# Kernel tuning notes

Hardware: AMD Instinct MI355X
Metric: run time of the kernel (lower is better)

## Reference

```python
import jax, jax.numpy as jnp
import numpy as np

B = 2
E = [16384, 32768, 65536, 131072]
CONVS = [256, 128, 64, 32, 8]


def mesh_conv(x, gemm, W, b):
    # x: (B, C, E); gemm: (E, 4) neighbor edge indices; W: (Cout, Cin, 5)
    n = x[:, :, gemm]  # (B, C, E, 4) irregular gather over mesh topology
    f1, f2, f3, f4 = n[..., 0], n[..., 1], n[..., 2], n[..., 3]
    # MeshCNN symmetric functions over the 4 gemm neighbors
    G = jnp.stack([x, f1 + f3, f2 + f4, jnp.abs(f1 - f3), jnp.abs(f2 - f4)], axis=-1)  # (B,C,E,5)
    return jnp.einsum('bces,ocs->boe', G, W) + b[None, :, None]


def inorm(x, eps=1e-5):
    # InstanceNorm2d, affine=False: normalize per (sample, channel) over edge dim
    m = jnp.mean(x, axis=2, keepdims=True)
    v = jnp.var(x, axis=2, keepdims=True)
    return (x - m) * jax.lax.rsqrt(v + eps)


def setup_inputs() -> dict:
    key = jax.random.key(0)
    ks = iter(jax.random.split(key, 64))
    inp = {}
    inp['fe'] = jax.random.normal(next(ks), (B, CONVS[0], E[0]), jnp.float32)
    for i in range(3):
        inp[f'skip{i}'] = jax.random.normal(next(ks), (B, CONVS[i + 1], E[i + 1]), jnp.float32)
    for r in range(4):
        inp[f'gemm{r}'] = jax.random.randint(next(ks), (E[r], 4), 0, E[r], jnp.int32)
    for i in range(3):
        inp[f'unpool{i}'] = jax.random.randint(next(ks), (E[i + 1],), 0, E[i], jnp.int32)

    def mk(cout, cin, name):
        inp[f'W{name}'] = jax.random.normal(next(ks), (cout, cin, 5), jnp.float32) * (1.0 / np.sqrt(5.0 * cin))
        inp[f'b{name}'] = jnp.zeros((cout,), jnp.float32)

    for i in range(3):
        mk(CONVS[i + 1], CONVS[i], f'up{i}')
        mk(CONVS[i + 1], CONVS[i + 1], f'c{i}')
    mk(CONVS[4], CONVS[3], 'upf')
    mk(CONVS[4], CONVS[4], 'cf')
    return inp


def reference(fe, skip0, skip1, skip2, gemm0, gemm1, gemm2, gemm3,
              unpool0, unpool1, unpool2,
              Wup0, bup0, Wc0, bc0, Wup1, bup1, Wc1, bc1, Wup2, bup2, Wc2, bc2,
              Wupf, bupf, Wcf, bcf):
    gemms = [gemm0, gemm1, gemm2, gemm3]
    unpools = [unpool0, unpool1, unpool2]
    skips = [skip0, skip1, skip2]
    Wups = [Wup0, Wup1, Wup2]
    bups = [bup0, bup1, bup2]
    Wcs = [Wc0, Wc1, Wc2]
    bcs = [bc0, bc1, bc2]
    x = fe
    for i in range(3):  # fixed small loop over decoder stages
        x1 = mesh_conv(x, gemms[i], Wups[i], bups[i])      # up_conv at coarse res
        x1 = x1[:, :, unpools[i]]                          # MeshUnpool: copy to fine edges
        x1 = x1 + skips[i]                                 # transfer_data skip add
        x1 = mesh_conv(x1, gemms[i + 1], Wcs[i], bcs[i])   # conv1 at fine res
        x = jax.nn.relu(inorm(x1))                         # InstanceNorm + ReLU (blocks=0)
    # final UpConv: no unroll, no skip
    x1 = mesh_conv(x, gemms[3], Wupf, bupf)
    x1 = mesh_conv(x1, gemms[3], Wcf, bcf)
    return jax.nn.relu(inorm(x1))
```

## Files before the change

kernel.cpp:

```cpp
#include <hip/hip_runtime.h>
#include <hip/hip_bf16.h>
#include <cstdint>
#include <cstddef>


typedef short s16x8 __attribute__((ext_vector_type(8)));
typedef unsigned short u16x8 __attribute__((ext_vector_type(8)));
typedef float f32x4 __attribute__((ext_vector_type(4)));

__device__ __forceinline__ float bfbits2f(unsigned short u) {
    unsigned int x = ((unsigned int)u) << 16;
    float f; __builtin_memcpy(&f, &x, sizeof(f)); return f;
}
__device__ __forceinline__ unsigned short f2bfbits(float f) {
    __hip_bfloat16 h = __float2bfloat16(f);
    unsigned short u; __builtin_memcpy(&u, &h, sizeof(u)); return u;
}

__global__ __launch_bounds__(256) void k_transpose_in(
    const float* __restrict__ in, unsigned short* __restrict__ out, int C, int E)
{
    __shared__ float tile[64][65];
    const int e0 = blockIdx.x * 64;
    const int c0 = blockIdx.y * 64;
    const int b  = blockIdx.z;
    const float* inb = in + (size_t)b * C * E;
    const int l = threadIdx.x % 64;
    const int g = threadIdx.x / 64;
#pragma unroll
    for (int i = 0; i < 16; ++i) {
        const int c = i * 4 + g;
        tile[c][l] = inb[(size_t)(c0 + c) * E + e0 + l];
    }
    __syncthreads();
    unsigned short* outb = out + (size_t)b * E * C;
#pragma unroll
    for (int i = 0; i < 16; ++i) {
        const int e = i * 4 + g;
        outb[(size_t)(e0 + e) * C + c0 + l] = f2bfbits(tile[l][e]);
    }
}

__global__ __launch_bounds__(256) void k_prep_b(
    const float* __restrict__ W, unsigned short* __restrict__ Bp, int C, int OP, int OL)
{
    const int p = blockIdx.x * 256 + threadIdx.x;
    const int total = 5 * C * OP;
    if (p >= total) return;
    const int j = p & 7;
    const int t = p >> 3;
    const int o = t % OP;
    const int kk = t / OP;
    const int k = kk * 8 + j;
    const int s = k / C;
    const int c = k - s * C;
    Bp[p] = (o < OL) ? f2bfbits(W[((size_t)o * C + c) * 5 + s]) : (unsigned short)0;
}

__global__ __launch_bounds__(256) void k_prep_w(
    const float* __restrict__ W, float* __restrict__ Wt, int C, int O)
{
    const int idx = blockIdx.x * 256 + threadIdx.x;
    const int total = C * 5 * O;
    if (idx >= total) return;
    const int k = idx / O;
    const int o = idx % O;
    const int c = k / 5;
    const int s = k - 5 * c;
    Wt[idx] = W[((size_t)o * C + c) * 5 + s];
}

template<int C, int O, bool STATS, int OW = O>
__global__ __launch_bounds__(256) void k_conv_mfma(
    const unsigned short* __restrict__ x, const int* __restrict__ gm,
    const unsigned short* __restrict__ Bp, const float* __restrict__ bias,
    unsigned short* __restrict__ out, float* __restrict__ stats, int E)
{
    constexpr int NT    = O / 16;
    constexpr int ITS   = C / 32;
    constexpr int OCT   = C / 8;
    constexpr int ITERS = (64 * OCT) / 256;
    constexpr int PAD   = 8;
    constexpr int RW    = C + PAD;
    constexpr bool PAIRED = (C <= 128);
    constexpr int SLOTS = PAIRED ? 2 : 1;
    static_assert(C % 32 == 0 && O % 16 == 0, "bad cfg");

    __shared__ unsigned short smem[SLOTS][64][RW];
    __shared__ int gis[64][4];

    const int tid  = threadIdx.x;
    const int wave = tid >> 6;
    const int lane = tid & 63;
    const int m    = lane & 15;
    const int kq   = lane >> 4;
    const int b    = blockIdx.y;
    const int e0   = blockIdx.x * 64;
    const unsigned short* xb = x + (size_t)b * E * C;
    const s16x8* Bp8 = reinterpret_cast<const s16x8*>(Bp);

    if (tid < 64)
        *reinterpret_cast<int4*>(gis[tid]) =
            *reinterpret_cast<const int4*>(gm + 4 * (size_t)(e0 + tid));

    f32x4 acc[NT];
#pragma unroll
    for (int nt = 0; nt < NT; ++nt) acc[nt] = (f32x4){0.f, 0.f, 0.f, 0.f};

    auto mfma_seg = [&](int slot, int s) {
#pragma unroll
        for (int it = 0; it < ITS; ++it) {
            const s16x8 afrag = *reinterpret_cast<const s16x8*>(
                &smem[slot][wave * 16 + m][it * 32 + kq * 8]);
            const int kkb = s * OCT + it * 4 + kq;
#pragma unroll
            for (int nt = 0; nt < NT; ++nt) {
                const s16x8 bfrag = Bp8[(size_t)kkb * O + nt * 16 + m];
                acc[nt] = __builtin_amdgcn_mfma_f32_16x16x32_bf16(afrag, bfrag, acc[nt], 0, 0, 0);
            }
        }
    };

#pragma unroll
    for (int i = 0; i < ITERS; ++i) {
        const int task = i * 256 + tid;
        const int r    = task / OCT;
        const int oct  = task % OCT;
        const u16x8 v = *reinterpret_cast<const u16x8*>(
            xb + (size_t)(e0 + r) * C + oct * 8);
        *reinterpret_cast<u16x8*>(&smem[0][r][oct * 8]) = v;
    }
    __syncthreads();
    mfma_seg(0, 0);
    __syncthreads();

    if constexpr (PAIRED) {
#pragma unroll
        for (int i = 0; i < ITERS; ++i) {
            const int task = i * 256 + tid;
            const int r    = task / OCT;
            const int oct  = task % OCT;
            const u16x8 a = *reinterpret_cast<const u16x8*>(
                xb + (size_t)gis[r][0] * C + oct * 8);
            const u16x8 c = *reinterpret_cast<const u16x8*>(
                xb + (size_t)gis[r][2] * C + oct * 8);
            u16x8 vs, vd;
#pragma unroll
            for (int j = 0; j < 8; ++j) {
                const float fa = bfbits2f(a[j]);
                const float fc = bfbits2f(c[j]);
                vs[j] = f2bfbits(fa + fc);
                vd[j] = f2bfbits(fabsf(fa - fc));
            }
            *reinterpret_cast<u16x8*>(&smem[0][r][oct * 8]) = vs;
            *reinterpret_cast<u16x8*>(&smem[SLOTS - 1][r][oct * 8]) = vd;
        }
        __syncthreads();
        mfma_seg(0, 1);
        mfma_seg(SLOTS - 1, 3);
        __syncthreads();
#pragma unroll
        for (int i = 0; i < ITERS; ++i) {
            const int task = i * 256 + tid;
            const int r    = task / OCT;
            const int oct  = task % OCT;
            const u16x8 a = *reinterpret_cast<const u16x8*>(
                xb + (size_t)gis[r][1] * C + oct * 8);
            const u16x8 c = *reinterpret_cast<const u16x8*>(
                xb + (size_t)gis[r][3] * C + oct * 8);
            u16x8 vs, vd;
#pragma unroll
            for (int j = 0; j < 8; ++j) {
                const float fa = bfbits2f(a[j]);
                const float fc = bfbits2f(c[j]);
                vs[j] = f2bfbits(fa + fc);
                vd[j] = f2bfbits(fabsf(fa - fc));
            }
            *reinterpret_cast<u16x8*>(&smem[0][r][oct * 8]) = vs;
            *reinterpret_cast<u16x8*>(&smem[SLOTS - 1][r][oct * 8]) = vd;
        }
        __syncthreads();
        mfma_seg(0, 2);
        mfma_seg(SLOTS - 1, 4);
    } else {
#pragma unroll
        for (int s = 1; s <= 4; ++s) {
            const int ia = (s == 1 || s == 3) ? 0 : 1;
#pragma unroll
            for (int i = 0; i < ITERS; ++i) {
                const int task = i * 256 + tid;
                const int r    = task / OCT;
                const int oct  = task % OCT;
                const u16x8 a = *reinterpret_cast<const u16x8*>(
                    xb + (size_t)gis[r][ia] * C + oct * 8);
                const u16x8 c = *reinterpret_cast<const u16x8*>(
                    xb + (size_t)gis[r][ia + 2] * C + oct * 8);
                u16x8 v;
#pragma unroll
                for (int j = 0; j < 8; ++j) {
                    const float fa = bfbits2f(a[j]);
                    const float fc = bfbits2f(c[j]);
                    v[j] = f2bfbits((s < 3) ? (fa + fc) : fabsf(fa - fc));
                }
                *reinterpret_cast<u16x8*>(&smem[0][r][oct * 8]) = v;
            }
            __syncthreads();
            mfma_seg(0, s);
            if (s != 4) __syncthreads();
        }
    }

    const int ebase = e0 + wave * 16 + kq * 4;
    float ssum[NT], ssq[NT];
#pragma unroll
    for (int nt = 0; nt < NT; ++nt) { ssum[nt] = 0.f; ssq[nt] = 0.f; }
#pragma unroll
    for (int nt = 0; nt < NT; ++nt) {
        const int o = nt * 16 + m;
        if (o < OW) {
            const float bo = bias[o];
#pragma unroll
            for (int r = 0; r < 4; ++r) {
                const float z = acc[nt][r] + bo;
                out[((size_t)b * E + (ebase + r)) * OW + o] = f2bfbits(z);
                ssum[nt] += z; ssq[nt] += z * z;
            }
        }
    }

    if constexpr (STATS) {
        __shared__ float ls[4][2][O];
#pragma unroll
        for (int nt = 0; nt < NT; ++nt) {
            float s = ssum[nt], q = ssq[nt];
            s += __shfl_xor(s, 16); s += __shfl_xor(s, 32);
            q += __shfl_xor(q, 16); q += __shfl_xor(q, 32);
            if (kq == 0) { ls[wave][0][nt * 16 + m] = s; ls[wave][1][nt * 16 + m] = q; }
        }
        __syncthreads();
        if (tid < O) {
            const float S = ls[0][0][tid] + ls[1][0][tid] + ls[2][0][tid] + ls[3][0][tid];
            const float Q = ls[0][1][tid] + ls[1][1][tid] + ls[2][1][tid] + ls[3][1][tid];
            atomicAdd(&stats[((size_t)b * O + tid) * 2], S);
            atomicAdd(&stats[((size_t)b * O + tid) * 2 + 1], Q);
        }
    }
}

template<int C, int O, bool STATS>
__global__ __launch_bounds__(256) void k_conv_small(
    const unsigned short* __restrict__ x, const int* __restrict__ gm,
    const float* __restrict__ Wt, const float* __restrict__ bias,
    unsigned short* __restrict__ out, float* __restrict__ stats, int E)
{
    static_assert(O == 8 && C % 8 == 0, "bad cfg");
    __shared__ float ls[2 * O];
    const int tid = threadIdx.x;
    if constexpr (STATS) {
        if (tid < 2 * O) ls[tid] = 0.f;
        __syncthreads();
    }
    const int b = blockIdx.y;
    const int e = blockIdx.x * 256 + tid;
    const unsigned short* xb = x + (size_t)b * E * C;
    const int4 gi = *reinterpret_cast<const int4*>(gm + 4 * (size_t)e);
    const unsigned short* rp[5] = {
        xb + (size_t)e * C, xb + (size_t)gi.x * C, xb + (size_t)gi.y * C,
        xb + (size_t)gi.z * C, xb + (size_t)gi.w * C };

    float acc[O];
#pragma unroll
    for (int o = 0; o < O; ++o) acc[o] = bias[o];

#pragma unroll
    for (int c = 0; c < C; c += 8) {
        u16x8 rv[5];
#pragma unroll
        for (int k = 0; k < 5; ++k) rv[k] = *reinterpret_cast<const u16x8*>(rp[k] + c);
#pragma unroll
        for (int cc = 0; cc < 8; ++cc) {
            const float x0 = bfbits2f(rv[0][cc]);
            const float f1 = bfbits2f(rv[1][cc]);
            const float f2 = bfbits2f(rv[2][cc]);
            const float f3 = bfbits2f(rv[3][cc]);
            const float f4 = bfbits2f(rv[4][cc]);
            const float gv[5] = { x0, f1 + f3, f2 + f4, fabsf(f1 - f3), fabsf(f2 - f4) };
            const float* wbase = Wt + (size_t)(c + cc) * 5 * O;
#pragma unroll
            for (int s = 0; s < 5; ++s)
#pragma unroll
                for (int o = 0; o < O; ++o)
                    acc[o] += gv[s] * wbase[s * O + o];
        }
    }

    u16x8 ov;
#pragma unroll
    for (int o = 0; o < O; ++o) ov[o] = f2bfbits(acc[o]);
    *reinterpret_cast<u16x8*>(out + ((size_t)b * E + e) * O) = ov;

    if constexpr (STATS) {
#pragma unroll
        for (int o = 0; o < O; ++o) {
            atomicAdd(&ls[o * 2], acc[o]);
            atomicAdd(&ls[o * 2 + 1], acc[o] * acc[o]);
        }
        __syncthreads();
        if (tid < 2 * O) atomicAdd(&stats[(size_t)b * 2 * O + tid], ls[tid]);
    }
}

template<int O>
__global__ __launch_bounds__(256) void k_unpool_skip(
    const unsigned short* __restrict__ y, const int* __restrict__ up,
    const float* __restrict__ skip, unsigned short* __restrict__ out,
    int Ein, int Eout)
{
    __shared__ float sk[O][65];
    const int b  = blockIdx.y;
    const int e0 = blockIdx.x * 64;
    const int t  = threadIdx.x;
    constexpr int L = O / 16;
#pragma unroll
    for (int i = 0; i < L; ++i) {
        const int flat = i * 256 + t;
        const int o = flat >> 4;
        const int el4 = (flat & 15) * 4;
        const float4 v = *reinterpret_cast<const float4*>(
            skip + ((size_t)b * O + o) * Eout + e0 + el4);
        sk[o][el4]     = v.x;
        sk[o][el4 + 1] = v.y;
        sk[o][el4 + 2] = v.z;
        sk[o][el4 + 3] = v.w;
    }
    __syncthreads();
    constexpr int OG  = O / 4;
    constexpr int EPP = 256 / OG;
    const int o4  = (t % OG) * 4;
    const int elg = t / OG;
#pragma unroll
    for (int p = 0; p < 64 / EPP; ++p) {
        const int el = p * EPP + elg;
        const int e  = e0 + el;
        const int u  = up[e];
        const ushort4 yv = *reinterpret_cast<const ushort4*>(
            y + ((size_t)b * Ein + u) * O + o4);
        ushort4 ov;
        ov.x = f2bfbits(bfbits2f(yv.x) + sk[o4 + 0][el]);
        ov.y = f2bfbits(bfbits2f(yv.y) + sk[o4 + 1][el]);
        ov.z = f2bfbits(bfbits2f(yv.z) + sk[o4 + 2][el]);
        ov.w = f2bfbits(bfbits2f(yv.w) + sk[o4 + 3][el]);
        *reinterpret_cast<ushort4*>(out + ((size_t)b * Eout + e) * O + o4) = ov;
    }
}

__global__ __launch_bounds__(256) void k_scale(
    const float* __restrict__ stats, float* __restrict__ ss, int BC, float invE)
{
    const int t = threadIdx.x;
    if (t < BC) {
        const float sum = stats[t * 2];
        const float sq  = stats[t * 2 + 1];
        const float m   = sum * invE;
        const float var = fmaxf(sq * invE - m * m, 0.f);
        const float sc  = rsqrtf(var + 1e-5f);
        ss[t * 2] = sc;
        ss[t * 2 + 1] = -m * sc;
    }
}

template<int C>
__global__ __launch_bounds__(256) void k_norm_relu(
    unsigned short* __restrict__ x, const float* __restrict__ ss, int E)
{
    const int b = blockIdx.y;
    const size_t i8 = ((size_t)blockIdx.x * 256 + threadIdx.x) * 8;
    const int c0 = (int)(i8 % C);
    unsigned short* p = x + (size_t)b * E * C + i8;
    const u16x8 v = *reinterpret_cast<const u16x8*>(p);
    u16x8 r;
#pragma unroll
    for (int j = 0; j < 8; ++j) {
        const float sc = ss[(b * C + c0 + j) * 2];
        const float sh = ss[(b * C + c0 + j) * 2 + 1];
        r[j] = f2bfbits(fmaxf(bfbits2f(v[j]) * sc + sh, 0.f));
    }
    *reinterpret_cast<u16x8*>(p) = r;
}

__global__ __launch_bounds__(256) void k_final_out(
    const unsigned short* __restrict__ z, const float* __restrict__ ss,
    float* __restrict__ out, int E)
{
    const int b = blockIdx.y;
    const int idx = blockIdx.x * 256 + threadIdx.x;
    const int o = idx / E;
    const int e = idx % E;
    const float sc = ss[((size_t)b * 8 + o) * 2];
    const float sh = ss[((size_t)b * 8 + o) * 2 + 1];
    const float v = bfbits2f(z[((size_t)b * E + e) * 8 + o]) * sc + sh;
    out[(size_t)b * 8 * E + idx] = fmaxf(v, 0.f);
}

extern "C" void kernel_launch(void* const* d_in, const int* in_sizes, int n_in,
                              void* d_out, int out_size, void* d_ws, size_t ws_size,
                              hipStream_t stream)
{
    (void)in_sizes; (void)n_in; (void)out_size; (void)ws_size;

    const float* fe = (const float*)d_in[0];
    const int* gemm0 = (const int*)d_in[4];
    const int* gemm1 = (const int*)d_in[5];
    const int* gemm2 = (const int*)d_in[6];
    const int* gemm3 = (const int*)d_in[7];
    const int* up0 = (const int*)d_in[8];
    const int* up1 = (const int*)d_in[9];
    const int* up2 = (const int*)d_in[10];
    const float* bup0 = (const float*)d_in[12];
    const float* bc0  = (const float*)d_in[14];
    const float* bup1 = (const float*)d_in[16];
    const float* bc1  = (const float*)d_in[18];
    const float* bup2 = (const float*)d_in[20];
    const float* bc2  = (const float*)d_in[22];
    const float* bupf = (const float*)d_in[24];
    const float* bcf  = (const float*)d_in[26];

    unsigned short* wsb = (unsigned short*)d_ws;
    const size_t NP = 8388608;
    unsigned short* P0 = wsb;
    unsigned short* P1 = wsb + NP;
    unsigned short* P2 = wsb + 2 * NP;
    unsigned short* Bp_up0 = wsb + 3 * NP;
    unsigned short* Bp_c0  = Bp_up0 + 163840;
    unsigned short* Bp_up1 = Bp_c0  + 81920;
    unsigned short* Bp_c1  = Bp_up1 + 40960;
    unsigned short* Bp_up2 = Bp_c1  + 20480;
    unsigned short* Bp_c2  = Bp_up2 + 10240;
    unsigned short* Bp_upf = Bp_c2  + 5120;
    float* fls    = (float*)(Bp_upf + 2560);
    float* wt_cf  = fls;
    float* stats0 = wt_cf  + 320;
    float* stats1 = stats0 + 512;
    float* stats2 = stats1 + 256;
    float* stats3 = stats2 + 128;
    float* ss0    = stats3 + 32;
    float* ss1    = ss0 + 512;
    float* ss2    = ss1 + 256;
    float* ss3    = ss2 + 128;

    hipMemsetAsync(stats0, 0, 928 * sizeof(float), stream);

    const dim3 blk(256);

    k_transpose_in<<<dim3(16384 / 64, 256 / 64, 2), blk, 0, stream>>>(fe, P0, 256, 16384);

    k_prep_b<<<dim3(163840 / 256), blk, 0, stream>>>((const float*)d_in[11], Bp_up0, 256, 128, 128);
    k_prep_b<<<dim3(81920 / 256),  blk, 0, stream>>>((const float*)d_in[13], Bp_c0, 128, 128, 128);
    k_prep_b<<<dim3(40960 / 256),  blk, 0, stream>>>((const float*)d_in[15], Bp_up1, 128, 64, 64);
    k_prep_b<<<dim3(20480 / 256),  blk, 0, stream>>>((const float*)d_in[17], Bp_c1, 64, 64, 64);
    k_prep_b<<<dim3(10240 / 256),  blk, 0, stream>>>((const float*)d_in[19], Bp_up2, 64, 32, 32);
    k_prep_b<<<dim3(5120 / 256),   blk, 0, stream>>>((const float*)d_in[21], Bp_c2, 32, 32, 32);
    k_prep_b<<<dim3(2560 / 256),   blk, 0, stream>>>((const float*)d_in[23], Bp_upf, 32, 16, 8);
    k_prep_w<<<dim3((320 + 255) / 256), blk, 0, stream>>>((const float*)d_in[25], wt_cf, 8, 8);

    k_conv_mfma<256, 128, false><<<dim3(16384 / 64, 2), blk, 0, stream>>>(P0, gemm0, Bp_up0, bup0, P1, nullptr, 16384);
    k_unpool_skip<128><<<dim3(32768 / 64, 2), blk, 0, stream>>>(P1, up0, (const float*)d_in[1], P2, 16384, 32768);
    k_conv_mfma<128, 128, true><<<dim3(32768 / 64, 2), blk, 0, stream>>>(P2, gemm1, Bp_c0, bc0, P0, stats0, 32768);
    k_scale<<<dim3(1), blk, 0, stream>>>(stats0, ss0, 256, 1.f / 32768.f);
    k_norm_relu<128><<<dim3(32768 * 128 / 2048, 2), blk, 0, stream>>>(P0, ss0, 32768);

    k_conv_mfma<128, 64, false><<<dim3(32768 / 64, 2), blk, 0, stream>>>(P0, gemm1, Bp_up1, bup1, P1, nullptr, 32768);
    k_unpool_skip<64><<<dim3(65536 / 64, 2), blk, 0, stream>>>(P1, up1, (const float*)d_in[2], P2, 32768, 65536);
    k_conv_mfma<64, 64, true><<<dim3(65536 / 64, 2), blk, 0, stream>>>(P2, gemm2, Bp_c1, bc1, P0, stats1, 65536);
    k_scale<<<dim3(1), blk, 0, stream>>>(stats1, ss1, 128, 1.f / 65536.f);
    k_norm_relu<64><<<dim3(65536 * 64 / 2048, 2), blk, 0, stream>>>(P0, ss1, 65536);

    k_conv_mfma<64, 32, false><<<dim3(65536 / 64, 2), blk, 0, stream>>>(P0, gemm2, Bp_up2, bup2, P1, nullptr, 65536);
    k_unpool_skip<32><<<dim3(131072 / 64, 2), blk, 0, stream>>>(P1, up2, (const float*)d_in[3], P2, 65536, 131072);
    k_conv_mfma<32, 32, true><<<dim3(131072 / 64, 2), blk, 0, stream>>>(P2, gemm3, Bp_c2, bc2, P0, stats2, 131072);
    k_scale<<<dim3(1), blk, 0, stream>>>(stats2, ss2, 64, 1.f / 131072.f);
    k_norm_relu<32><<<dim3(131072 * 32 / 2048, 2), blk, 0, stream>>>(P0, ss2, 131072);

    k_conv_mfma<32, 16, false, 8><<<dim3(131072 / 64, 2), blk, 0, stream>>>(P0, gemm3, Bp_upf, bupf, P1, nullptr, 131072);
    k_conv_small<8, 8, true><<<dim3(131072 / 256, 2), blk, 0, stream>>>(P1, gemm3, wt_cf, bcf, P2, stats3, 131072);
    k_scale<<<dim3(1), blk, 0, stream>>>(stats3, ss3, 16, 1.f / 131072.f);
    k_final_out<<<dim3(8 * 131072 / 256, 2), blk, 0, stream>>>(P2, ss3, (float*)d_out, 131072);
}
```

Measured before the change: 743.1 us.

## Load own-edge A fragments directly to registers and batch all gathers for small C

The self-feature segment is now loaded straight from global memory into per-lane MFMA A fragments, skipping the shared-memory staging pass and one barrier pair. For C<=64 all four neighbour gathers are issued at once into four shared slots, so a single barrier precedes all five MFMA segments. Gather indices are read as one int4 from shared memory. This trades more shared memory and registers (occupancy risk) for fewer synchronisations and more memory-level parallelism in the gather.

```diff
diff --git a/kernel.cpp b/kernel.cpp
--- a/kernel.cpp
+++ b/kernel.cpp
@@ -82,11 +82,10 @@
     constexpr int ITERS = (64 * OCT) / 256;
     constexpr int PAD   = 8;
     constexpr int RW    = C + PAD;
-    constexpr bool PAIRED = (C <= 128);
-    constexpr int SLOTS = PAIRED ? 2 : 1;
+    constexpr int NSLOT = (C <= 64) ? 4 : (C == 128) ? 2 : 1;
     static_assert(C % 32 == 0 && O % 16 == 0, "bad cfg");
 
-    __shared__ unsigned short smem[SLOTS][64][RW];
+    __shared__ unsigned short smem[NSLOT][64][RW];
     __shared__ int gis[64][4];
 
     const int tid  = threadIdx.x;
@@ -102,11 +101,30 @@
     if (tid < 64)
         *reinterpret_cast<int4*>(gis[tid]) =
             *reinterpret_cast<const int4*>(gm + 4 * (size_t)(e0 + tid));
+    __syncthreads();
+
+    s16x8 a0[ITS];
+    {
+        const unsigned short* myrow = xb + (size_t)(e0 + wave * 16 + m) * C;
+#pragma unroll
+        for (int it = 0; it < ITS; ++it)
+            a0[it] = *reinterpret_cast<const s16x8*>(myrow + it * 32 + kq * 8);
+    }
 
     f32x4 acc[NT];
 #pragma unroll
     for (int nt = 0; nt < NT; ++nt) acc[nt] = (f32x4){0.f, 0.f, 0.f, 0.f};
 
+    auto mfma_own = [&]() {
+#pragma unroll
+        for (int it = 0; it < ITS; ++it) {
+            const int kkb = it * 4 + kq;
+#pragma unroll
+            for (int nt = 0; nt < NT; ++nt)
+                acc[nt] = __builtin_amdgcn_mfma_f32_16x16x32_bf16(
+                    a0[it], Bp8[(size_t)kkb * O + nt * 16 + m], acc[nt], 0, 0, 0);
+        }
+    };
     auto mfma_seg = [&](int slot, int s) {
 #pragma unroll
         for (int it = 0; it < ITS; ++it) {
@@ -114,74 +132,83 @@
                 &smem[slot][wave * 16 + m][it * 32 + kq * 8]);
             const int kkb = s * OCT + it * 4 + kq;
 #pragma unroll
-            for (int nt = 0; nt < NT; ++nt) {
-                const s16x8 bfrag = Bp8[(size_t)kkb * O + nt * 16 + m];
-                acc[nt] = __builtin_amdgcn_mfma_f32_16x16x32_bf16(afrag, bfrag, acc[nt], 0, 0, 0);
-            }
+            for (int nt = 0; nt < NT; ++nt)
+                acc[nt] = __builtin_amdgcn_mfma_f32_16x16x32_bf16(
+                    afrag, Bp8[(size_t)kkb * O + nt * 16 + m], acc[nt], 0, 0, 0);
         }
     };
 
-#pragma unroll
-    for (int i = 0; i < ITERS; ++i) {
-        const int task = i * 256 + tid;
-        const int r    = task / OCT;
-        const int oct  = task % OCT;
-        const u16x8 v = *reinterpret_cast<const u16x8*>(
-            xb + (size_t)(e0 + r) * C + oct * 8);
-        *reinterpret_cast<u16x8*>(&smem[0][r][oct * 8]) = v;
-    }
-    __syncthreads();
-    mfma_seg(0, 0);
-    __syncthreads();
-
-    if constexpr (PAIRED) {
+    if constexpr (C <= 64) {
 #pragma unroll
         for (int i = 0; i < ITERS; ++i) {
             const int task = i * 256 + tid;
             const int r    = task / OCT;
             const int oct  = task % OCT;
-            const u16x8 a = *reinterpret_cast<const u16x8*>(
-                xb + (size_t)gis[r][0] * C + oct * 8);
-            const u16x8 c = *reinterpret_cast<const u16x8*>(
-                xb + (size_t)gis[r][2] * C + oct * 8);
-            u16x8 vs, vd;
+            const int off  = oct * 8;
+            const int4 gi = *reinterpret_cast<const int4*>(gis[r]);
+            const u16x8 f1 = *reinterpret_cast<const u16x8*>(xb + (size_t)gi.x * C + off);
+            const u16x8 f3 = *reinterpret_cast<const u16x8*>(xb + (size_t)gi.z * C + off);
+            const u16x8 f2 = *reinterpret_cast<const u16x8*>(xb + (size_t)gi.y * C + off);
+            const u16x8 f4 = *reinterpret_cast<const u16x8*>(xb + (size_t)gi.w * C + off);
+            u16x8 vs13, vd13, vs24, vd24;
 #pragma unroll
             for (int j = 0; j < 8; ++j) {
-                const float fa = bfbits2f(a[j]);
-                const float fc = bfbits2f(c[j]);
-                vs[j] = f2bfbits(fa + fc);
-                vd[j] = f2bfbits(fabsf(fa - fc));
+                const float a1 = bfbits2f(f1[j]), a3 = bfbits2f(f3[j]);
+                const float a2 = bfbits2f(f2[j]), a4 = bfbits2f(f4[j]);
+                vs13[j] = f2bfbits(a1 + a3);
+                vd13[j] = f2bfbits(fabsf(a1 - a3));
+                vs24[j] = f2bfbits(a2 + a4);
+                vd24[j] = f2bfbits(fabsf(a2 - a4));
             }
-            *reinterpret_cast<u16x8*>(&smem[0][r][oct * 8]) = vs;
-            *reinterpret_cast<u16x8*>(&smem[SLOTS - 1][r][oct * 8]) = vd;
-        }
-        __syncthreads();
-        mfma_seg(0, 1);
-        mfma_seg(SLOTS - 1, 3);
-        __syncthreads();
+            *reinterpret_cast<u16x8*>(&smem[0][r][off]) = vs13;
+            *reinterpret_cast<u16x8*>(&smem[1][r][off]) = vd13;
+            *reinterpret_cast<u16x8*>(&smem[2][r][off]) = vs24;
+            *reinterpret_cast<u16x8*>(&smem[3][r][off]) = vd24;
+        }
+        __syncthreads();
+        mfma_own();
+        mfma_seg(0, 1); mfma_seg(1, 3); mfma_seg(2, 2); mfma_seg(3, 4);
+    } else if constexpr (C == 128) {
 #pragma unroll
         for (int i = 0; i < ITERS; ++i) {
             const int task = i * 256 + tid;
-            const int r    = task / OCT;
-            const int oct  = task % OCT;
-            const u16x8 a = *reinterpret_cast<const u16x8*>(
-                xb + (size_t)gis[r][1] * C + oct * 8);
-            const u16x8 c = *reinterpret_cast<const u16x8*>(
-                xb + (size_t)gis[r][3] * C + oct * 8);
+            const int r = task / OCT, oct = task % OCT, off = oct * 8;
+            const int4 gi = *reinterpret_cast<const int4*>(gis[r]);
+            const u16x8 f1 = *reinterpret_cast<const u16x8*>(xb + (size_t)gi.x * C + off);
+            const u16x8 f3 = *reinterpret_cast<const u16x8*>(xb + (size_t)gi.z * C + off);
             u16x8 vs, vd;
 #pragma unroll
             for (int j = 0; j < 8; ++j) {
-                const float fa = bfbits2f(a[j]);
-                const float fc = bfbits2f(c[j]);
-                vs[j] = f2bfbits(fa + fc);
-                vd[j] = f2bfbits(fabsf(fa - fc));
+                const float a1 = bfbits2f(f1[j]), a3 = bfbits2f(f3[j]);
+                vs[j] = f2bfbits(a1 + a3);
+                vd[j] = f2bfbits(fabsf(a1 - a3));
             }
-            *reinterpret_cast<u16x8*>(&smem[0][r][oct * 8]) = vs;
-            *reinterpret_cast<u16x8*>(&smem[SLOTS - 1][r][oct * 8]) = vd;
-        }
-        __syncthreads();
-        mfma_seg(0, 2);
-        mfma_seg(SLOTS - 1, 4);
+            *reinterpret_cast<u16x8*>(&smem[0][r][off]) = vs;
+            *reinterpret_cast<u16x8*>(&smem[1][r][off]) = vd;
+        }
+        __syncthreads();
+        mfma_own();
+        mfma_seg(0, 1); mfma_seg(1, 3);
+        __syncthreads();
+#pragma unroll
+        for (int i = 0; i < ITERS; ++i) {
+            const int task = i * 256 + tid;
+            const int r = task / OCT, oct = task % OCT, off = oct * 8;
+            const int4 gi = *reinterpret_cast<const int4*>(gis[r]);
+            const u16x8 f2 = *reinterpret_cast<const u16x8*>(xb + (size_t)gi.y * C + off);
+            const u16x8 f4 = *reinterpret_cast<const u16x8*>(xb + (size_t)gi.w * C + off);
+            u16x8 vs, vd;
+#pragma unroll
+            for (int j = 0; j < 8; ++j) {
+                const float a2 = bfbits2f(f2[j]), a4 = bfbits2f(f4[j]);
+                vs[j] = f2bfbits(a2 + a4);
+                vd[j] = f2bfbits(fabsf(a2 - a4));
+            }
+            *reinterpret_cast<u16x8*>(&smem[0][r][off]) = vs;
+            *reinterpret_cast<u16x8*>(&smem[1][r][off]) = vd;
+        }
+        __syncthreads();
+        mfma_seg(0, 2); mfma_seg(1, 4);
     } else {
 #pragma unroll
         for (int s = 1; s <= 4; ++s) {
@@ -189,12 +216,12 @@
 #pragma unroll
             for (int i = 0; i < ITERS; ++i) {
                 const int task = i * 256 + tid;
-                const int r    = task / OCT;
-                const int oct  = task % OCT;
-                const u16x8 a = *reinterpret_cast<const u16x8*>(
-                    xb + (size_t)gis[r][ia] * C + oct * 8);
-                const u16x8 c = *reinterpret_cast<const u16x8*>(
-                    xb + (size_t)gis[r][ia + 2] * C + oct * 8);
+                const int r = task / OCT, oct = task % OCT, off = oct * 8;
+                const int4 gi = *reinterpret_cast<const int4*>(gis[r]);
+                const int ra = (ia == 0) ? gi.x : gi.y;
+                const int rc = (ia == 0) ? gi.z : gi.w;
+                const u16x8 a = *reinterpret_cast<const u16x8*>(xb + (size_t)ra * C + off);
+                const u16x8 c = *reinterpret_cast<const u16x8*>(xb + (size_t)rc * C + off);
                 u16x8 v;
 #pragma unroll
                 for (int j = 0; j < 8; ++j) {
@@ -202,9 +229,10 @@
                     const float fc = bfbits2f(c[j]);
                     v[j] = f2bfbits((s < 3) ? (fa + fc) : fabsf(fa - fc));
                 }
-                *reinterpret_cast<u16x8*>(&smem[0][r][oct * 8]) = v;
+                *reinterpret_cast<u16x8*>(&smem[0][r][off]) = v;
             }
             __syncthreads();
+            if (s == 1) mfma_own();
             mfma_seg(0, s);
             if (s != 4) __syncthreads();
         }
```

New measurement: 723.5 us. 1.03x faster.
